# Performance work log

Hardware: AMD Instinct MI355X
Metric: run time of the kernel (lower is better)

## Reference

```python
import jax, jax.numpy as jnp
import numpy as np

B, Q, K = 16, 64, 1024
QS = KS = VS = 256
H = 128
NEG = -1e6


def setup_inputs() -> dict:
    key = jax.random.key(0)
    ks = jax.random.split(key, 7)
    queries = jax.random.normal(ks[0], (B, Q, QS), dtype=jnp.float32)
    keys = jax.random.normal(ks[1], (B, K, KS), dtype=jnp.float32)
    values = jax.random.normal(ks[2], (B, K, VS), dtype=jnp.float32)
    valid_len = jax.random.randint(ks[3], (B,), 0, 512, dtype=jnp.int64)
    # Linear weights (PyTorch Linear stores (out, in); we store (in, out) for x @ W)
    Wq = jax.random.normal(ks[4], (QS, H), dtype=jnp.float32) / np.sqrt(QS)
    Wk = jax.random.normal(ks[5], (KS, H), dtype=jnp.float32) / np.sqrt(KS)
    Ws = jax.random.normal(ks[6], (H,), dtype=jnp.float32) / np.sqrt(H)
    return {"queries": queries, "keys": keys, "values": values,
            "valid_len": valid_len, "Wq": Wq, "Wk": Wk, "Ws": Ws}


def reference(queries, keys, values, valid_len, Wq, Wk, Ws):
    q = jnp.einsum('bqe,eh->bqh', queries, Wq)          # (B,Q,H)
    k = jnp.einsum('bke,eh->bkh', keys, Wk)             # (B,K,H)
    features = jnp.tanh(q[:, :, None, :] + k[:, None, :, :])  # (B,Q,K,H)
    scores = jnp.einsum('bqkh,h->bqk', features, Ws)    # (B,Q,K)
    # front_mask=True: mask the FIRST valid_len[b] key positions
    pos = jnp.arange(K)
    valid = pos[None, None, :] >= valid_len[:, None, None]  # (B,1,K)
    scores = jnp.where(valid, scores, NEG)
    attn = jax.nn.softmax(scores, axis=-1)              # (B,Q,K)
    return jnp.einsum('bqk,bkv->bqv', attn, values)     # (B,Q,VS)
```

## Files before the change

### kernel.cpp

```cpp
#include <hip/hip_runtime.h>

#define NB 16
#define NQ 64
#define NK 1024
#define ES 256
#define NH 128
#define VS 256
#define KT 16
#define SCALE2 2.885390081777927f
#define L2E    1.4426950408889634f

__device__ __forceinline__ float exp2_fast(float x) {
    float r; asm("v_exp_f32 %0, %1" : "=v"(r) : "v"(x)); return r;
}
__device__ __forceinline__ float rcp_fast(float x) {
    float r; asm("v_rcp_f32 %0, %1" : "=v"(r) : "v"(x)); return r;
}
__device__ __forceinline__ void fma4(float4& acc, const float4& wv, float s) {
    acc.x = fmaf(wv.x, s, acc.x);
    acc.y = fmaf(wv.y, s, acc.y);
    acc.z = fmaf(wv.z, s, acc.z);
    acc.w = fmaf(wv.w, s, acc.w);
}

__global__ __launch_bounds__(256) void proj_kernel(
    const float* __restrict__ queries, const float* __restrict__ keys,
    const float* __restrict__ Wq, const float* __restrict__ Wk,
    float* __restrict__ qp, float* __restrict__ kp)
{
    __shared__ __align__(16) float x_lds[16 * 256];
    const int bi  = blockIdx.x;
    const int tid = threadIdx.x;

    const float* src; const float* W; float* dst;
    if (bi < 64) {
        src = queries + (size_t)bi * 16 * ES;
        W   = Wq;
        dst = qp + (size_t)bi * 16 * NH;
    } else {
        const int r0 = (bi - 64) * 16;
        src = keys + (size_t)r0 * ES;
        W   = Wk;
        dst = kp + (size_t)r0 * NH;
    }

    const float4* s4 = (const float4*)src;
    float4* x4 = (float4*)x_lds;
#pragma unroll
    for (int i = 0; i < 4; ++i) x4[tid + i * 256] = s4[tid + i * 256];
    __syncthreads();

    const int h4 = tid & 31;
    const int g  = tid >> 5;
    const float* xa = x_lds + (g + 0) * 256;
    const float* xb = x_lds + (g + 8) * 256;

    float4 a0 = {0,0,0,0}, a1 = {0,0,0,0};
#pragma unroll 4
    for (int e = 0; e < 256; e += 4) {
        const float4 va = *(const float4*)(xa + e);
        const float4 vb = *(const float4*)(xb + e);
#pragma unroll
        for (int j = 0; j < 4; ++j) {
            const float4 w4 = *(const float4*)(W + (size_t)(e + j) * NH + h4 * 4);
            const float fa = (j==0)?va.x:(j==1)?va.y:(j==2)?va.z:va.w;
            const float fb = (j==0)?vb.x:(j==1)?vb.y:(j==2)?vb.z:vb.w;
            fma4(a0, w4, fa);
            fma4(a1, w4, fb);
        }
    }
    const float c = SCALE2;
    float4 o;
    o.x=a0.x*c; o.y=a0.y*c; o.z=a0.z*c; o.w=a0.w*c;
    *(float4*)(dst + (size_t)(g + 0) * NH + h4 * 4) = o;
    o.x=a1.x*c; o.y=a1.y*c; o.z=a1.z*c; o.w=a1.w*c;
    *(float4*)(dst + (size_t)(g + 8) * NH + h4 * 4) = o;
}

__global__ __launch_bounds__(256, 4) void scores_kernel(
    const float* __restrict__ qp, const float* __restrict__ kp,
    const float* __restrict__ Ws, const int* __restrict__ valid_len,
    float* __restrict__ pT)
{
    __shared__ __align__(16) float kp_s[64 * 128];
    __shared__ __align__(16) float qp_s[8 * 128];
    __shared__ __align__(16) float ws_s[128];

    const int kt  = blockIdx.x;
    const int qt  = blockIdx.y;
    const int b   = blockIdx.z;
    const int tid = threadIdx.x;
    const int lane = tid & 63;
    const int w    = tid >> 6;
    const int kg   = kt * 64 + lane;
    const int vl   = valid_len[b];

    if (kt * 64 + 63 < vl) {
        pT[((size_t)b * NK + kg) * NQ + qt * 8 + w]     = 0.0f;
        pT[((size_t)b * NK + kg) * NQ + qt * 8 + w + 4] = 0.0f;
        return;
    }

    const float4* ksrc = (const float4*)(kp + (size_t)(b * NK + kt * 64) * NH);
#pragma unroll
    for (int i = 0; i < 8; ++i) {
        const int idx = tid + i * 256;
        const int row = idx >> 5, c = idx & 31;
        const float4 v = ksrc[idx];
        *(float4*)(kp_s + row * 128 + 4 * (c ^ (row & 7))) = v;
    }
    ((float4*)qp_s)[tid & 255] = ((const float4*)(qp + (size_t)(b * NQ + qt * 8) * NH))[tid & 255];
    if (tid < 32) {
        float4 t = ((const float4*)Ws)[tid];
        t.x *= -2.f; t.y *= -2.f; t.z *= -2.f; t.w *= -2.f;
        ((float4*)ws_s)[tid] = t;
    }
    __syncthreads();

    float sw = ws_s[lane] + ws_s[lane + 64];
#pragma unroll
    for (int off = 32; off; off >>= 1) sw += __shfl_xor(sw, off);
    const float sW = -0.5f * sw;

    const float* qa = qp_s + w * 128;
    const float* qb = qp_s + (w + 4) * 128;
    const float* kr = kp_s + lane * 128;
    const int sw_x = lane & 7;

    float s0 = 0.f, s1 = 0.f;
#pragma unroll 4
    for (int c = 0; c < 32; ++c) {
        const float4 kv = *(const float4*)(kr + 4 * (c ^ sw_x));
        const float4 va = *(const float4*)(qa + 4 * c);
        const float4 vb = *(const float4*)(qb + 4 * c);
        const float4 wv = *(const float4*)(ws_s + 4 * c);
        {
            const float u0 = 1.0f + exp2_fast(va.x + kv.x);
            const float u1 = 1.0f + exp2_fast(va.y + kv.y);
            const float u2 = 1.0f + exp2_fast(va.z + kv.z);
            const float u3 = 1.0f + exp2_fast(va.w + kv.w);
            const float d01 = u0 * u1, d23 = u2 * u3;
            const float n01 = fmaf(wv.y, u0, wv.x * u1);
            const float n23 = fmaf(wv.w, u2, wv.z * u3);
            const float n   = fmaf(n23, d01, n01 * d23);
            s0 = fmaf(n, rcp_fast(d01 * d23), s0);
        }
        {
            const float u0 = 1.0f + exp2_fast(vb.x + kv.x);
            const float u1 = 1.0f + exp2_fast(vb.y + kv.y);
            const float u2 = 1.0f + exp2_fast(vb.z + kv.z);
            const float u3 = 1.0f + exp2_fast(vb.w + kv.w);
            const float d01 = u0 * u1, d23 = u2 * u3;
            const float n01 = fmaf(wv.y, u0, wv.x * u1);
            const float n23 = fmaf(wv.w, u2, wv.z * u3);
            const float n   = fmaf(n23, d01, n01 * d23);
            s1 = fmaf(n, rcp_fast(d01 * d23), s1);
        }
    }

    const float p0 = (kg >= vl) ? exp2_fast((sW + s0) * L2E) : 0.0f;
    const float p1 = (kg >= vl) ? exp2_fast((sW + s1) * L2E) : 0.0f;
    pT[((size_t)b * NK + kg) * NQ + qt * 8 + w]     = p0;
    pT[((size_t)b * NK + kg) * NQ + qt * 8 + w + 4] = p1;
}

__global__ __launch_bounds__(256) void pv_kernel(
    const float* __restrict__ pT, const float* __restrict__ values,
    const int* __restrict__ valid_len,
    float* __restrict__ part, float* __restrict__ zpart)
{
    __shared__ __align__(16) float a_s[64][36];
    __shared__ float zp_s[4][32];
    const int kt  = blockIdx.x;
    const int qh  = blockIdx.y;
    const int b   = blockIdx.z;
    const int tid = threadIdx.x;

    const int vl = valid_len[b];
    if (kt * 64 + 63 < vl) {
        if (tid < 32) zpart[((size_t)kt * NB + b) * NQ + qh * 32 + tid] = 0.f;
#pragma unroll
        for (int q = 0; q < 32; ++q)
            part[(((size_t)kt * NB + b) * NQ + qh * 32 + q) * VS + tid] = 0.f;
        return;
    }

    {
        const int q4 = (tid & 7) * 4;
        const int k0 = tid >> 3;
#pragma unroll
        for (int i = 0; i < 2; ++i) {
            const int k = k0 + 32 * i;
            const float4 v = *(const float4*)(
                pT + ((size_t)b * NK + kt * 64 + k) * NQ + qh * 32 + q4);
            *(float4*)(&a_s[k][q4]) = v;
        }
    }
    __syncthreads();

    {
        const int lane = tid & 63;
        const int w    = tid >> 6;
        const int qq   = lane & 31;
        float z = 0.f;
#pragma unroll
        for (int i = 0; i < 16; ++i) z += a_s[w * 16 + i][qq];
        if (lane < 32) zp_s[w][qq] = z;
    }
    __syncthreads();
    if (tid < 32) {
        const float zf = zp_s[0][tid] + zp_s[1][tid] + zp_s[2][tid] + zp_s[3][tid];
        zpart[((size_t)kt * NB + b) * NQ + qh * 32 + tid] = zf;
    }

    float acc[32];
#pragma unroll
    for (int i = 0; i < 32; ++i) acc[i] = 0.f;

    const float* vb = values + ((size_t)b * NK + kt * 64) * VS + tid;
#pragma unroll 4
    for (int k = 0; k < 64; ++k) {
        const float v = vb[(size_t)k * VS];
#pragma unroll
        for (int j = 0; j < 8; ++j) {
            const float4 a = *(const float4*)(&a_s[k][4 * j]);
            acc[4*j+0] = fmaf(a.x, v, acc[4*j+0]);
            acc[4*j+1] = fmaf(a.y, v, acc[4*j+1]);
            acc[4*j+2] = fmaf(a.z, v, acc[4*j+2]);
            acc[4*j+3] = fmaf(a.w, v, acc[4*j+3]);
        }
    }
#pragma unroll
    for (int q = 0; q < 32; ++q)
        part[(((size_t)kt * NB + b) * NQ + qh * 32 + q) * VS + tid] = acc[q];
}

__global__ __launch_bounds__(256) void finish_kernel(
    const float* __restrict__ part, const float* __restrict__ zpart,
    float* __restrict__ out)
{
    const int r   = blockIdx.x;
    const int tid = threadIdx.x;
    const int b = r >> 6, q = r & 63;
    float z = 0.f, s = 0.f;
#pragma unroll
    for (int kt = 0; kt < KT; ++kt) {
        z += zpart[((size_t)kt * NB + b) * NQ + q];
        s += part[(((size_t)kt * NB + b) * NQ + q) * VS + tid];
    }
    out[(size_t)r * VS + tid] = s / z;
}

extern "C" void kernel_launch(void* const* d_in, const int* in_sizes, int n_in,
                              void* d_out, int out_size, void* d_ws, size_t ws_size,
                              hipStream_t stream)
{
    (void)in_sizes; (void)n_in; (void)out_size; (void)ws_size;
    const float* queries = (const float*)d_in[0];
    const float* keys    = (const float*)d_in[1];
    const float* values  = (const float*)d_in[2];
    const int*   vlen    = (const int*)d_in[3];
    const float* Wq      = (const float*)d_in[4];
    const float* Wk      = (const float*)d_in[5];
    const float* Ws      = (const float*)d_in[6];
    float* out = (float*)d_out;

    float* qp    = (float*)d_ws;
    float* kp    = qp + 131072;
    float* pT    = kp + 2097152;
    float* zpart = pT + 1048576;
    float* part  = zpart + 16384;

    proj_kernel<<<1088, 256, 0, stream>>>(queries, keys, Wq, Wk, qp, kp);
    scores_kernel<<<dim3(16, 8, 16), 256, 0, stream>>>(qp, kp, Ws, vlen, pT);
    pv_kernel<<<dim3(KT, 2, 16), 256, 0, stream>>>(pT, values, vlen, part, zpart);
    finish_kernel<<<1024, 256, 0, stream>>>(part, zpart, out);
}
```

Baseline: 170.0 us.

## Stage projection weights in double-buffered LDS and compute 32 rows per block

The projection kernel now loads 32 input rows per block instead of 16, which halves the grid. It streams the weight matrix through a double-buffered LDS tile, prefetching the next 32-row chunk into registers while computing on the current one. Each thread keeps four row accumulators, so every weight read is reused across more rows and global weight traffic per output drops. In exchange the block uses more LDS and registers and adds a barrier per chunk. This only touches the projection stage, which is a small part of the total pipeline.

```diff
diff --git a/kernel.cpp b/kernel.cpp
--- a/kernel.cpp
+++ b/kernel.cpp
@@ -23,58 +23,101 @@
     acc.w = fmaf(wv.w, s, acc.w);
 }
 
-__global__ __launch_bounds__(256) void proj_kernel(
+__global__ __launch_bounds__(256, 2) void proj_kernel(
     const float* __restrict__ queries, const float* __restrict__ keys,
     const float* __restrict__ Wq, const float* __restrict__ Wk,
     float* __restrict__ qp, float* __restrict__ kp)
 {
-    __shared__ __align__(16) float x_lds[16 * 256];
+    __shared__ __align__(16) float x_lds[32 * 256];
+    __shared__ __align__(16) float w_lds[2][32 * 128];
     const int bi  = blockIdx.x;
     const int tid = threadIdx.x;
 
     const float* src; const float* W; float* dst;
-    if (bi < 64) {
-        src = queries + (size_t)bi * 16 * ES;
+    if (bi < 32) {
+        src = queries + (size_t)bi * 32 * ES;
         W   = Wq;
-        dst = qp + (size_t)bi * 16 * NH;
+        dst = qp + (size_t)bi * 32 * NH;
     } else {
-        const int r0 = (bi - 64) * 16;
+        const int r0 = (bi - 32) * 32;
         src = keys + (size_t)r0 * ES;
         W   = Wk;
         dst = kp + (size_t)r0 * NH;
     }
 
-    const float4* s4 = (const float4*)src;
-    float4* x4 = (float4*)x_lds;
-#pragma unroll
-    for (int i = 0; i < 4; ++i) x4[tid + i * 256] = s4[tid + i * 256];
+    {
+        const float4* s4 = (const float4*)src;
+        float4* x4 = (float4*)x_lds;
+#pragma unroll
+        for (int i = 0; i < 8; ++i) x4[tid + i * 256] = s4[tid + i * 256];
+        const float4* w4p = (const float4*)W;
+        float4* wb = (float4*)w_lds[0];
+#pragma unroll
+        for (int j = 0; j < 4; ++j) wb[tid + j * 256] = w4p[tid + j * 256];
+    }
     __syncthreads();
 
     const int h4 = tid & 31;
     const int g  = tid >> 5;
-    const float* xa = x_lds + (g + 0) * 256;
-    const float* xb = x_lds + (g + 8) * 256;
-
-    float4 a0 = {0,0,0,0}, a1 = {0,0,0,0};
-#pragma unroll 4
-    for (int e = 0; e < 256; e += 4) {
-        const float4 va = *(const float4*)(xa + e);
-        const float4 vb = *(const float4*)(xb + e);
-#pragma unroll
-        for (int j = 0; j < 4; ++j) {
-            const float4 w4 = *(const float4*)(W + (size_t)(e + j) * NH + h4 * 4);
-            const float fa = (j==0)?va.x:(j==1)?va.y:(j==2)?va.z:va.w;
-            const float fb = (j==0)?vb.x:(j==1)?vb.y:(j==2)?vb.z:vb.w;
-            fma4(a0, w4, fa);
-            fma4(a1, w4, fb);
-        }
-    }
-    const float c = SCALE2;
+    const float* xr0 = x_lds + (g +  0) * 256;
+    const float* xr1 = x_lds + (g +  8) * 256;
+    const float* xr2 = x_lds + (g + 16) * 256;
+    const float* xr3 = x_lds + (g + 24) * 256;
+
+    float4 a0 = {0,0,0,0}, a1 = {0,0,0,0}, a2 = {0,0,0,0}, a3 = {0,0,0,0};
+
+    int cur = 0;
+#pragma unroll 1
+    for (int c = 0; c < 8; ++c) {
+        const int kc = c * 32;
+        float4 t0 = {0,0,0,0}, t1 = {0,0,0,0}, t2 = {0,0,0,0}, t3 = {0,0,0,0};
+        if (c < 7) {
+            const float4* w4p = (const float4*)(W + (size_t)(kc + 32) * NH);
+            t0 = w4p[tid + 0 * 256];
+            t1 = w4p[tid + 1 * 256];
+            t2 = w4p[tid + 2 * 256];
+            t3 = w4p[tid + 3 * 256];
+        }
+        const float* wc = w_lds[cur];
+#pragma unroll
+        for (int e4 = 0; e4 < 8; ++e4) {
+            const int e = kc + e4 * 4;
+            const float4 va = *(const float4*)(xr0 + e);
+            const float4 vb = *(const float4*)(xr1 + e);
+            const float4 vc = *(const float4*)(xr2 + e);
+            const float4 vd = *(const float4*)(xr3 + e);
+#pragma unroll
+            for (int j = 0; j < 4; ++j) {
+                const float4 w4 = *(const float4*)(wc + (e4 * 4 + j) * 128 + h4 * 4);
+                const float fa = (j==0)?va.x:(j==1)?va.y:(j==2)?va.z:va.w;
+                const float fb = (j==0)?vb.x:(j==1)?vb.y:(j==2)?vb.z:vb.w;
+                const float fc = (j==0)?vc.x:(j==1)?vc.y:(j==2)?vc.z:vc.w;
+                const float fd = (j==0)?vd.x:(j==1)?vd.y:(j==2)?vd.z:vd.w;
+                fma4(a0, w4, fa); fma4(a1, w4, fb);
+                fma4(a2, w4, fc); fma4(a3, w4, fd);
+            }
+        }
+        if (c < 7) {
+            float4* wn = (float4*)w_lds[cur ^ 1];
+            wn[tid + 0 * 256] = t0;
+            wn[tid + 1 * 256] = t1;
+            wn[tid + 2 * 256] = t2;
+            wn[tid + 3 * 256] = t3;
+        }
+        __syncthreads();
+        cur ^= 1;
+    }
+
+    const float cc = SCALE2;
     float4 o;
-    o.x=a0.x*c; o.y=a0.y*c; o.z=a0.z*c; o.w=a0.w*c;
-    *(float4*)(dst + (size_t)(g + 0) * NH + h4 * 4) = o;
-    o.x=a1.x*c; o.y=a1.y*c; o.z=a1.z*c; o.w=a1.w*c;
-    *(float4*)(dst + (size_t)(g + 8) * NH + h4 * 4) = o;
+    o.x=a0.x*cc; o.y=a0.y*cc; o.z=a0.z*cc; o.w=a0.w*cc;
+    *(float4*)(dst + (size_t)(g +  0) * NH + h4 * 4) = o;
+    o.x=a1.x*cc; o.y=a1.y*cc; o.z=a1.z*cc; o.w=a1.w*cc;
+    *(float4*)(dst + (size_t)(g +  8) * NH + h4 * 4) = o;
+    o.x=a2.x*cc; o.y=a2.y*cc; o.z=a2.z*cc; o.w=a2.w*cc;
+    *(float4*)(dst + (size_t)(g + 16) * NH + h4 * 4) = o;
+    o.x=a3.x*cc; o.y=a3.y*cc; o.z=a3.z*cc; o.w=a3.w*cc;
+    *(float4*)(dst + (size_t)(g + 24) * NH + h4 * 4) = o;
 }
 
 __global__ __launch_bounds__(256, 4) void scores_kernel(
@@ -271,7 +314,7 @@
     float* zpart = pT + 1048576;
     float* part  = zpart + 16384;
 
-    proj_kernel<<<1088, 256, 0, stream>>>(queries, keys, Wq, Wk, qp, kp);
+    proj_kernel<<<544, 256, 0, stream>>>(queries, keys, Wq, Wk, qp, kp);
     scores_kernel<<<dim3(16, 8, 16), 256, 0, stream>>>(qp, kp, Ws, vlen, pT);
     pv_kernel<<<dim3(KT, 2, 16), 256, 0, stream>>>(pT, values, vlen, part, zpart);
     finish_kernel<<<1024, 256, 0, stream>>>(part, zpart, out);
```

New measurement: 200.9 us. +18.2%, slower.
